# Kernel optimization log

Hardware: AMD Instinct MI355X
Metric: run time of the kernel (lower is better)

## Reference

```python
import jax, jax.numpy as jnp
import numpy as np

N, E = 100000, 1600000
IN_DIM, H, D = 128, 4, 32
ALPHA = 0.2  # leaky relu negative slope


def setup_inputs() -> dict:
    key = jax.random.key(0)
    k1, k2, k3, k4, k5, k6 = jax.random.split(key, 6)
    return {
        "inputs": jax.random.normal(k1, (N, IN_DIM), dtype=jnp.float32),
        "src": jax.random.randint(k2, (E,), 0, N, dtype=jnp.int32),
        "dst": jax.random.randint(k3, (E,), 0, N, dtype=jnp.int32),
        "fc_w": jax.random.normal(k4, (IN_DIM, H * D), dtype=jnp.float32) * (1.414 / np.sqrt(IN_DIM)),
        "attn_l": jax.random.normal(k5, (D,), dtype=jnp.float32) * 0.1,
        "attn_r": jax.random.normal(k6, (D,), dtype=jnp.float32) * 0.1,
    }


def reference(inputs, src, dst, fc_w, attn_l, attn_r):
    # fc + reshape to (N, H, D); feat_drop is identity (p=0)
    ft = (inputs @ fc_w).reshape(N, H, D)
    # attn_l/attn_r are (1,1,D) in torch -> broadcast over heads
    a1 = jnp.einsum("nhd,d->nh", ft, attn_l)  # (N, H)
    a2 = jnp.einsum("nhd,d->nh", ft, attn_r)  # (N, H)
    # per-edge logits; original keeps ONLY head-0 scores after edge_softmax
    # (scores[:, 0, :].unsqueeze(1)), so we only need head 0 here.
    e = jax.nn.leaky_relu(a1[src, 0] + a2[dst, 0], ALPHA)  # (E,)
    # numerically-stable segment softmax over destination nodes
    emax = jax.ops.segment_max(e, dst, num_segments=N)
    ex = jnp.exp(e - emax[dst])
    denom = jax.ops.segment_sum(ex, dst, num_segments=N)
    a = ex / denom[dst]  # (E,) broadcast to all heads
    # u_mul_e + sum aggregation; attn_drop is identity (p=0)
    msg = ft[src] * a[:, None, None]  # (E, H, D)
    out = jax.ops.segment_sum(msg, dst, num_segments=N)  # (N, H, D)
    return out
```

## Files before the change

kernel.cpp:

```cpp
#include <hip/hip_runtime.h>


#define ALPHA 0.2f
#define NBLK 512
#define BBITS 8
#define BSIZE 256
#define CAP 5120

typedef __attribute__((ext_vector_type(8))) short bf16x8;
typedef __attribute__((ext_vector_type(8))) unsigned short u16x8;
typedef __attribute__((ext_vector_type(4))) float f32x4;

__device__ __forceinline__ unsigned short f2bf(float f) {
    unsigned u = __float_as_uint(f);
    unsigned r = (u + 0x7FFFu + ((u >> 16) & 1u)) >> 16;
    return (unsigned short)r;
}

__global__ __launch_bounds__(256) void prep_kernel(const float* __restrict__ W,
                                                   u16x8* __restrict__ Wswz) {
    int gt = blockIdx.x * 256 + threadIdx.x;
    if (gt < 2048) {
        int n = gt >> 4, c = gt & 15;
        u16x8 v;
        #pragma unroll
        for (int j = 0; j < 8; ++j) v[j] = f2bf(W[(c * 8 + j) * 128 + n]);
        Wswz[n * 16 + (c ^ (n & 7))] = v;
    }
}

__global__ __launch_bounds__(256) void front_kernel(
        const float* __restrict__ A, const u16x8* __restrict__ Wswz,
        const float* __restrict__ attn_l, const float* __restrict__ attn_r,
        unsigned short* __restrict__ ftb,
        float* __restrict__ s_l, float* __restrict__ s_r, int N, int GB,
        const int* __restrict__ dst, unsigned* __restrict__ bh,
        int E, int nbucket, int slice) {
    __shared__ char smem[49152];
    const int tid = threadIdx.x;

    if (blockIdx.x >= (unsigned)GB) {
        unsigned* cnt = (unsigned*)smem;
        for (int i = tid; i < nbucket; i += 256) cnt[i] = 0u;
        __syncthreads();
        const int b = blockIdx.x - GB;
        int s0 = b * slice, s1 = min(s0 + slice, E);
        for (int i = s0 + tid; i < s1; i += 256)
            atomicAdd(&cnt[((unsigned)dst[i]) >> BBITS], 1u);
        __syncthreads();
        for (int k = tid; k < nbucket; k += 256)
            bh[(size_t)k * NBLK + b] = cnt[k];
        return;
    }

    u16x8* A_lds = (u16x8*)smem;
    u16x8* W_lds = (u16x8*)(smem + 16384);
    const int block_row = blockIdx.x * 64;

    for (int i = tid; i < 2048; i += 256) W_lds[i] = Wswz[i];

    for (int l = tid; l < 1024; l += 256) {
        int m = l >> 4, c = l & 15;
        int row = block_row + m;
        float4 v0 = make_float4(0.f, 0.f, 0.f, 0.f), v1 = v0;
        if (row < N) {
            const float4* p = (const float4*)(A + (size_t)row * 128 + c * 8);
            v0 = p[0]; v1 = p[1];
        }
        u16x8 u;
        u[0] = f2bf(v0.x); u[1] = f2bf(v0.y); u[2] = f2bf(v0.z); u[3] = f2bf(v0.w);
        u[4] = f2bf(v1.x); u[5] = f2bf(v1.y); u[6] = f2bf(v1.z); u[7] = f2bf(v1.w);
        A_lds[m * 16 + (c ^ (m & 7))] = u;
    }
    __syncthreads();

    const int wv = tid >> 6;
    const int lane = tid & 63;
    const int lm = lane & 15;
    const int quad = lane >> 4;

    f32x4 acc[8];
    #pragma unroll
    for (int t = 0; t < 8; ++t) acc[t] = (f32x4)(0.f);

    const int am = wv * 16 + lm;
    #pragma unroll
    for (int ks = 0; ks < 4; ++ks) {
        int c = ks * 4 + quad;
        bf16x8 af = *(const bf16x8*)&A_lds[am * 16 + (c ^ (am & 7))];
        #pragma unroll
        for (int t = 0; t < 8; ++t) {
            int n = t * 16 + lm;
            bf16x8 bf = *(const bf16x8*)&W_lds[n * 16 + (c ^ (n & 7))];
            acc[t] = __builtin_amdgcn_mfma_f32_16x16x32_bf16(af, bf, acc[t], 0, 0, 0);
        }
    }

    {
        float al0 = attn_l[lm], al1 = attn_l[16 + lm];
        float ar0 = attn_r[lm], ar1 = attn_r[16 + lm];
        #pragma unroll
        for (int r = 0; r < 4; ++r) {
            float pl = acc[0][r] * al0 + acc[1][r] * al1;
            float pr = acc[0][r] * ar0 + acc[1][r] * ar1;
            #pragma unroll
            for (int mask = 1; mask < 16; mask <<= 1) {
                pl += __shfl_xor(pl, mask, 64);
                pr += __shfl_xor(pr, mask, 64);
            }
            if (lm == 0) {
                int row = block_row + wv * 16 + quad * 4 + r;
                if (row < N) { s_l[row] = pl; s_r[row] = pr; }
            }
        }
    }

    unsigned short* C_lds = (unsigned short*)A_lds;
    #pragma unroll
    for (int t = 0; t < 8; ++t) {
        #pragma unroll
        for (int r = 0; r < 4; ++r) {
            int mrow = wv * 16 + quad * 4 + r;
            C_lds[mrow * 128 + t * 16 + lm] = f2bf(acc[t][r]);
        }
    }
    __syncthreads();
    for (int l = tid; l < 1024; l += 256) {
        int m = l >> 4, c = l & 15;
        int row = block_row + m;
        if (row < N)
            *(u16x8*)(ftb + (size_t)row * 128 + c * 8) = *(const u16x8*)&C_lds[m * 128 + c * 8];
    }
}

__global__ __launch_bounds__(256) void scan1_kernel(const unsigned* __restrict__ counts,
                                                    unsigned* __restrict__ S,
                                                    unsigned* __restrict__ partials, int M) {
    __shared__ unsigned sh[256];
    const int tid = threadIdx.x;
    const int base = blockIdx.x * 1024 + tid * 4;
    unsigned v[4];
    unsigned s = 0;
    #pragma unroll
    for (int k = 0; k < 4; ++k) {
        int idx = base + k;
        v[k] = (idx < M) ? counts[idx] : 0u;
        s += v[k];
    }
    sh[tid] = s;
    __syncthreads();
    for (int off = 1; off < 256; off <<= 1) {
        unsigned t = (tid >= off) ? sh[tid - off] : 0u;
        __syncthreads();
        sh[tid] += t;
        __syncthreads();
    }
    if (tid == 255) partials[blockIdx.x] = sh[255];
    unsigned run = (tid == 0) ? 0u : sh[tid - 1];
    #pragma unroll
    for (int k = 0; k < 4; ++k) {
        int idx = base + k;
        if (idx < M) S[idx] = run;
        run += v[k];
    }
}

__global__ __launch_bounds__(256) void scan2_kernel(unsigned* __restrict__ partials, int NB) {
    __shared__ unsigned sh[256];
    const int tid = threadIdx.x;
    unsigned v[4];
    unsigned s = 0;
    #pragma unroll
    for (int k = 0; k < 4; ++k) {
        int idx = tid * 4 + k;
        v[k] = (idx < NB) ? partials[idx] : 0u;
        s += v[k];
    }
    sh[tid] = s;
    __syncthreads();
    for (int off = 1; off < 256; off <<= 1) {
        unsigned t = (tid >= off) ? sh[tid - off] : 0u;
        __syncthreads();
        sh[tid] += t;
        __syncthreads();
    }
    unsigned run = (tid == 0) ? 0u : sh[tid - 1];
    #pragma unroll
    for (int k = 0; k < 4; ++k) {
        int idx = tid * 4 + k;
        if (idx < NB) partials[idx] = run;
        run += v[k];
    }
}

__global__ __launch_bounds__(256) void bscatter_kernel(
        const int* __restrict__ src, const int* __restrict__ dst,
        const float* __restrict__ s_l, const float* __restrict__ s_r,
        const unsigned* __restrict__ S, const unsigned* __restrict__ partials,
        uint2* __restrict__ staged, int E, int nbucket, int slice) {
    __shared__ unsigned basel[512];
    __shared__ unsigned cur[512];
    const int b = blockIdx.x;
    for (int k = threadIdx.x; k < nbucket; k += 256) {
        unsigned idx = (unsigned)k * NBLK + b;
        basel[k] = S[idx] + partials[idx >> 10];
        cur[k] = 0u;
    }
    __syncthreads();
    int s0 = b * slice, s1 = min(s0 + slice, E);
    for (int i = s0 + threadIdx.x; i < s1; i += 256) {
        int s = src[i], d = dst[i];
        unsigned k = ((unsigned)d) >> BBITS;
        float x = s_l[s] + s_r[d];
        float e = (x > 0.f) ? x : ALPHA * x;
        unsigned pos = basel[k] + atomicAdd(&cur[k], 1u);
        staged[pos] = make_uint2((unsigned)s | (((unsigned)d & (BSIZE - 1)) << 20),
                                 __float_as_uint(e));
    }
}

__global__ __launch_bounds__(256) void bsort_kernel(
        uint2* __restrict__ staged, const unsigned* __restrict__ S,
        const unsigned* __restrict__ partials,
        unsigned* __restrict__ offsets, int N, int E, int nbucket) {
    __shared__ uint2 rec[CAP];
    __shared__ unsigned cnt[BSIZE], incl[BSIZE], cur[BSIZE];
    const int k = blockIdx.x;
    const int t = threadIdx.x;
    unsigned idx0 = (unsigned)k * NBLK;
    unsigned gstart = S[idx0] + partials[idx0 >> 10];
    unsigned gend = (k + 1 == nbucket) ? (unsigned)E
                                       : (S[idx0 + NBLK] + partials[(idx0 + NBLK) >> 10]);
    int n = (int)(gend - gstart);
    if (n > CAP) n = CAP;

    cnt[t] = 0u;
    __syncthreads();
    for (int i = t; i < n; i += 256)
        atomicAdd(&cnt[staged[gstart + i].x >> 20], 1u);
    __syncthreads();
    incl[t] = cnt[t];
    __syncthreads();
    for (int off = 1; off < 256; off <<= 1) {
        unsigned u = (t >= off) ? incl[t - off] : 0u;
        __syncthreads();
        incl[t] += u;
        __syncthreads();
    }
    cur[t] = 0u;
    __syncthreads();
    for (int i = t; i < n; i += 256) {
        uint2 r = staged[gstart + i];
        unsigned dl = r.x >> 20;
        unsigned p = incl[dl] - cnt[dl] + atomicAdd(&cur[dl], 1u);
        rec[p] = r;
    }
    __syncthreads();
    int d = k * BSIZE + t;
    if (d < N) {
        int b0 = (int)(incl[t] - cnt[t]);
        int c = (int)cnt[t];
        float m = -1e30f;
        for (int j = 0; j < c; ++j) m = fmaxf(m, __uint_as_float(rec[b0 + j].y));
        float sum = 0.f;
        for (int j = 0; j < c; ++j) sum += __expf(__uint_as_float(rec[b0 + j].y) - m);
        float rden = (c > 0) ? 1.f / sum : 0.f;
        for (int j = 0; j < c; ++j) {
            float a = __expf(__uint_as_float(rec[b0 + j].y) - m) * rden;
            rec[b0 + j].y = __float_as_uint(a);
        }
        offsets[d] = gstart + incl[t];
    }
    __syncthreads();
    for (int i = t; i < n; i += 256) {
        uint2 r = rec[i];
        staged[gstart + i] = make_uint2(r.x & 0xFFFFFu, r.y);
    }
}

__global__ __launch_bounds__(256) void aggregate_kernel(
        const uint2* __restrict__ edata, const unsigned* __restrict__ offsets,
        const unsigned short* __restrict__ ftb, float* __restrict__ out, int N) {
    int wv = threadIdx.x >> 6;
    int lane = threadIdx.x & 63;
    int d = blockIdx.x * 4 + wv;
    if (d >= N) return;
    int eh = lane >> 4;
    int j  = lane & 15;

    unsigned start = (d == 0) ? 0u : offsets[d - 1];
    unsigned end = offsets[d];

    float acc[8] = {0.f, 0.f, 0.f, 0.f, 0.f, 0.f, 0.f, 0.f};
    for (unsigned e = start; e < end; e += 8) {
        unsigned i0 = e + eh, i1 = e + 4 + eh;
        uint2 d0 = (i0 < end) ? edata[i0] : make_uint2(0u, 0u);
        uint2 d1 = (i1 < end) ? edata[i1] : make_uint2(0u, 0u);
        uint4 q0 = *(const uint4*)(ftb + (size_t)d0.x * 128 + j * 8);
        uint4 q1 = *(const uint4*)(ftb + (size_t)d1.x * 128 + j * 8);
        float a0 = __uint_as_float(d0.y);
        float a1 = __uint_as_float(d1.y);
        const unsigned* w0 = (const unsigned*)&q0;
        const unsigned* w1 = (const unsigned*)&q1;
        #pragma unroll
        for (int p = 0; p < 4; ++p) {
            acc[2 * p]     += a0 * __uint_as_float(w0[p] << 16);
            acc[2 * p + 1] += a0 * __uint_as_float(w0[p] & 0xFFFF0000u);
            acc[2 * p]     += a1 * __uint_as_float(w1[p] << 16);
            acc[2 * p + 1] += a1 * __uint_as_float(w1[p] & 0xFFFF0000u);
        }
    }
    #pragma unroll
    for (int p = 0; p < 8; ++p) {
        acc[p] += __shfl_xor(acc[p], 16, 64);
        acc[p] += __shfl_xor(acc[p], 32, 64);
    }
    if (eh == 0) {
        float4* op = (float4*)(out + (size_t)d * 128 + j * 8);
        op[0] = make_float4(acc[0], acc[1], acc[2], acc[3]);
        op[1] = make_float4(acc[4], acc[5], acc[6], acc[7]);
    }
}

static inline size_t align256(size_t x) { return (x + 255) & ~(size_t)255; }

extern "C" void kernel_launch(void* const* d_in, const int* in_sizes, int n_in,
                              void* d_out, int out_size, void* d_ws, size_t ws_size,
                              hipStream_t stream) {
    const float* inputs = (const float*)d_in[0];
    const int*   src    = (const int*)d_in[1];
    const int*   dst    = (const int*)d_in[2];
    const float* fc_w   = (const float*)d_in[3];
    const float* attn_l = (const float*)d_in[4];
    const float* attn_r = (const float*)d_in[5];
    float* out = (float*)d_out;

    const int N = in_sizes[0] / 128;
    const int E = in_sizes[1];
    const int nbucket = (N + BSIZE - 1) / BSIZE;
    const int M = nbucket * NBLK;
    const int NB1 = (M + 1023) / 1024;
    const int slice = (E + NBLK - 1) / NBLK;
    const int GB = (N + 63) / 64;

    char* w = (char*)d_ws;
    unsigned short* ftb = (unsigned short*)w;  w += align256((size_t)N * 128 * 2);
    float*    s_l      = (float*)w;     w += align256((size_t)N * 4);
    float*    s_r      = (float*)w;     w += align256((size_t)N * 4);
    unsigned* bh       = (unsigned*)w;  w += align256((size_t)M * 4);
    unsigned* S        = (unsigned*)w;  w += align256((size_t)M * 4);
    unsigned* partials = (unsigned*)w;  w += align256(1024 * 4);
    unsigned* offsets  = (unsigned*)w;  w += align256((size_t)N * 4);
    u16x8*    Wswz     = (u16x8*)w;     w += align256(2048 * 16);
    uint2*    staged   = (uint2*)w;     w += align256((size_t)E * 8);

    prep_kernel<<<8, 256, 0, stream>>>(fc_w, Wswz);
    front_kernel<<<GB + NBLK, 256, 0, stream>>>(inputs, Wswz, attn_l, attn_r,
                                                ftb, s_l, s_r, N, GB,
                                                dst, bh, E, nbucket, slice);
    scan1_kernel<<<NB1, 256, 0, stream>>>(bh, S, partials, M);
    scan2_kernel<<<1, 256, 0, stream>>>(partials, NB1);
    bscatter_kernel<<<NBLK, 256, 0, stream>>>(src, dst, s_l, s_r, S, partials,
                                              staged, E, nbucket, slice);
    bsort_kernel<<<nbucket, 256, 0, stream>>>(staged, S, partials, offsets,
                                              N, E, nbucket);
    aggregate_kernel<<<(N + 3) / 4, 256, 0, stream>>>(staged, offsets, ftb, out, N);
}
```

Baseline: 252.1 us.

## Parallelize per-node softmax with shared atomics and stage edge data in LDS

The bucket sort kernel now computes the per-destination max and sum with shared-memory atomics (atomicMax on order-preserving float keys, atomicAdd on floats) over all threads. This replaces the serial per-thread loops whose cost scaled with node degree, and the kernel writes sorted normalized records directly. The aggregate kernel cooperatively loads each block's edge records into LDS and unrolls the gather loop to four edges per iteration, raising memory-level parallelism. The price is more shared-memory atomics, extra block-level syncs, and nondeterministic summation order.

Measured after the change: 259.0 us. +2.7%, slower.

```diff
diff --git a/kernel.cpp b/kernel.cpp
--- a/kernel.cpp
+++ b/kernel.cpp
@@ -6,6 +6,7 @@
 #define BBITS 8
 #define BSIZE 256
 #define CAP 5120
+#define ESLOTS 1024
 
 typedef __attribute__((ext_vector_type(8))) short bf16x8;
 typedef __attribute__((ext_vector_type(8))) unsigned short u16x8;
@@ -15,6 +16,14 @@
     unsigned u = __float_as_uint(f);
     unsigned r = (u + 0x7FFFu + ((u >> 16) & 1u)) >> 16;
     return (unsigned short)r;
+}
+
+__device__ __forceinline__ unsigned mkey(unsigned u) {
+    return ((int)u < 0) ? ~u : (u | 0x80000000u);
+}
+__device__ __forceinline__ float unmkey(unsigned k) {
+    unsigned u = ((int)k < 0) ? (k & 0x7FFFFFFFu) : ~k;
+    return __uint_as_float(u);
 }
 
 __global__ __launch_bounds__(256) void prep_kernel(const float* __restrict__ W,
@@ -224,7 +233,8 @@
         const unsigned* __restrict__ partials,
         unsigned* __restrict__ offsets, int N, int E, int nbucket) {
     __shared__ uint2 rec[CAP];
-    __shared__ unsigned cnt[BSIZE], incl[BSIZE], cur[BSIZE];
+    __shared__ unsigned cnt[BSIZE], incl[BSIZE], cur[BSIZE], mx[BSIZE];
+    __shared__ float sm[BSIZE];
     const int k = blockIdx.x;
     const int t = threadIdx.x;
     unsigned idx0 = (unsigned)k * NBLK;
@@ -235,9 +245,17 @@
     if (n > CAP) n = CAP;
 
     cnt[t] = 0u;
-    __syncthreads();
-    for (int i = t; i < n; i += 256)
-        atomicAdd(&cnt[staged[gstart + i].x >> 20], 1u);
+    cur[t] = 0u;
+    mx[t] = 0u;
+    sm[t] = 0.f;
+    __syncthreads();
+    for (int i = t; i < n; i += 256) {
+        uint2 r = staged[gstart + i];
+        rec[i] = r;
+        unsigned dl = r.x >> 20;
+        atomicAdd(&cnt[dl], 1u);
+        atomicMax(&mx[dl], mkey(r.y));
+    }
     __syncthreads();
     incl[t] = cnt[t];
     __syncthreads();
@@ -247,67 +265,84 @@
         incl[t] += u;
         __syncthreads();
     }
-    cur[t] = 0u;
-    __syncthreads();
-    for (int i = t; i < n; i += 256) {
-        uint2 r = staged[gstart + i];
-        unsigned dl = r.x >> 20;
-        unsigned p = incl[dl] - cnt[dl] + atomicAdd(&cur[dl], 1u);
-        rec[p] = r;
-    }
-    __syncthreads();
-    int d = k * BSIZE + t;
-    if (d < N) {
-        int b0 = (int)(incl[t] - cnt[t]);
-        int c = (int)cnt[t];
-        float m = -1e30f;
-        for (int j = 0; j < c; ++j) m = fmaxf(m, __uint_as_float(rec[b0 + j].y));
-        float sum = 0.f;
-        for (int j = 0; j < c; ++j) sum += __expf(__uint_as_float(rec[b0 + j].y) - m);
-        float rden = (c > 0) ? 1.f / sum : 0.f;
-        for (int j = 0; j < c; ++j) {
-            float a = __expf(__uint_as_float(rec[b0 + j].y) - m) * rden;
-            rec[b0 + j].y = __float_as_uint(a);
-        }
-        offsets[d] = gstart + incl[t];
-    }
-    __syncthreads();
     for (int i = t; i < n; i += 256) {
         uint2 r = rec[i];
-        staged[gstart + i] = make_uint2(r.x & 0xFFFFFu, r.y);
+        unsigned dl = r.x >> 20;
+        atomicAdd(&sm[dl], __expf(__uint_as_float(r.y) - unmkey(mx[dl])));
+    }
+    __syncthreads();
+    float ssum = sm[t];
+    sm[t] = (cnt[t] > 0) ? 1.f / ssum : 0.f;
+    int d = k * BSIZE + t;
+    if (d < N) offsets[d] = gstart + incl[t];
+    __syncthreads();
+    for (int i = t; i < n; i += 256) {
+        uint2 r = rec[i];
+        unsigned dl = r.x >> 20;
+        float a = __expf(__uint_as_float(r.y) - unmkey(mx[dl])) * sm[dl];
+        unsigned p = incl[dl] - cnt[dl] + atomicAdd(&cur[dl], 1u);
+        staged[gstart + p] = make_uint2(r.x & 0xFFFFFu, __float_as_uint(a));
     }
 }
 
 __global__ __launch_bounds__(256) void aggregate_kernel(
         const uint2* __restrict__ edata, const unsigned* __restrict__ offsets,
         const unsigned short* __restrict__ ftb, float* __restrict__ out, int N) {
-    int wv = threadIdx.x >> 6;
-    int lane = threadIdx.x & 63;
-    int d = blockIdx.x * 4 + wv;
-    if (d >= N) return;
-    int eh = lane >> 4;
-    int j  = lane & 15;
-
-    unsigned start = (d == 0) ? 0u : offsets[d - 1];
-    unsigned end = offsets[d];
+    __shared__ uint2 elds[ESLOTS];
+    const int wv = threadIdx.x >> 6;
+    const int lane = threadIdx.x & 63;
+    const int eh = lane >> 4;
+    const int j  = lane & 15;
+    const int db = blockIdx.x * 4;
+    const int d = db + wv;
+
+    const unsigned bstart = (db == 0) ? 0u : offsets[db - 1];
+    const unsigned bend = offsets[min(db + 3, N - 1)];
+    unsigned start = 0u, end = 0u;
+    if (d < N) {
+        start = (d == 0) ? 0u : offsets[d - 1];
+        end = offsets[d];
+    }
 
     float acc[8] = {0.f, 0.f, 0.f, 0.f, 0.f, 0.f, 0.f, 0.f};
-    for (unsigned e = start; e < end; e += 8) {
-        unsigned i0 = e + eh, i1 = e + 4 + eh;
-        uint2 d0 = (i0 < end) ? edata[i0] : make_uint2(0u, 0u);
-        uint2 d1 = (i1 < end) ? edata[i1] : make_uint2(0u, 0u);
-        uint4 q0 = *(const uint4*)(ftb + (size_t)d0.x * 128 + j * 8);
-        uint4 q1 = *(const uint4*)(ftb + (size_t)d1.x * 128 + j * 8);
-        float a0 = __uint_as_float(d0.y);
-        float a1 = __uint_as_float(d1.y);
-        const unsigned* w0 = (const unsigned*)&q0;
-        const unsigned* w1 = (const unsigned*)&q1;
-        #pragma unroll
-        for (int p = 0; p < 4; ++p) {
-            acc[2 * p]     += a0 * __uint_as_float(w0[p] << 16);
-            acc[2 * p + 1] += a0 * __uint_as_float(w0[p] & 0xFFFF0000u);
-            acc[2 * p]     += a1 * __uint_as_float(w1[p] << 16);
-            acc[2 * p + 1] += a1 * __uint_as_float(w1[p] & 0xFFFF0000u);
+
+    for (unsigned cbase = bstart; cbase < bend; cbase += ESLOTS) {
+        const unsigned cn = min((unsigned)ESLOTS, bend - cbase);
+        __syncthreads();
+        for (unsigned i = threadIdx.x; i < cn; i += 256)
+            elds[i] = edata[cbase + i];
+        __syncthreads();
+        const unsigned lo = (start > cbase) ? start : cbase;
+        const unsigned hi = (end < cbase + cn) ? end : (cbase + cn);
+        for (unsigned e = lo; e < hi; e += 16) {
+            unsigned i0 = e + eh, i1 = e + 4 + eh, i2 = e + 8 + eh, i3 = e + 12 + eh;
+            uint2 e0 = (i0 < hi) ? elds[i0 - cbase] : make_uint2(0u, 0u);
+            uint2 e1 = (i1 < hi) ? elds[i1 - cbase] : make_uint2(0u, 0u);
+            uint2 e2 = (i2 < hi) ? elds[i2 - cbase] : make_uint2(0u, 0u);
+            uint2 e3 = (i3 < hi) ? elds[i3 - cbase] : make_uint2(0u, 0u);
+            uint4 q0 = *(const uint4*)(ftb + (size_t)e0.x * 128 + j * 8);
+            uint4 q1 = *(const uint4*)(ftb + (size_t)e1.x * 128 + j * 8);
+            uint4 q2 = *(const uint4*)(ftb + (size_t)e2.x * 128 + j * 8);
+            uint4 q3 = *(const uint4*)(ftb + (size_t)e3.x * 128 + j * 8);
+            float a0 = __uint_as_float(e0.y);
+            float a1 = __uint_as_float(e1.y);
+            float a2 = __uint_as_float(e2.y);
+            float a3 = __uint_as_float(e3.y);
+            const unsigned* w0 = (const unsigned*)&q0;
+            const unsigned* w1 = (const unsigned*)&q1;
+            const unsigned* w2 = (const unsigned*)&q2;
+            const unsigned* w3 = (const unsigned*)&q3;
+            #pragma unroll
+            for (int p = 0; p < 4; ++p) {
+                acc[2 * p]     += a0 * __uint_as_float(w0[p] << 16);
+                acc[2 * p + 1] += a0 * __uint_as_float(w0[p] & 0xFFFF0000u);
+                acc[2 * p]     += a1 * __uint_as_float(w1[p] << 16);
+                acc[2 * p + 1] += a1 * __uint_as_float(w1[p] & 0xFFFF0000u);
+                acc[2 * p]     += a2 * __uint_as_float(w2[p] << 16);
+                acc[2 * p + 1] += a2 * __uint_as_float(w2[p] & 0xFFFF0000u);
+                acc[2 * p]     += a3 * __uint_as_float(w3[p] << 16);
+                acc[2 * p + 1] += a3 * __uint_as_float(w3[p] & 0xFFFF0000u);
+            }
         }
     }
     #pragma unroll
@@ -315,7 +350,7 @@
         acc[p] += __shfl_xor(acc[p], 16, 64);
         acc[p] += __shfl_xor(acc[p], 32, 64);
     }
-    if (eh == 0) {
+    if (d < N && eh == 0) {
         float4* op = (float4*)(out + (size_t)d * 128 + j * 8);
         op[0] = make_float4(acc[0], acc[1], acc[2], acc[3]);
         op[1] = make_float4(acc[4], acc[5], acc[6], acc[7]);
```
